# Performance work log

Measured on AMD Instinct MI355X. Metric: run time of the kernel, lower is better.

## Reference

```python
import jax, jax.numpy as jnp
import numpy as np

N = 131072          # source points
M = 65536           # sampled (query) points
NN = 32             # max_nr_neighbors
K = 15              # num_kernel_points
IN_F = 64
OUT_F = 128
MAP_SIZE = 40.0
SUB_DIST = 0.5      # subsampling_dist * subsampling_factor (meters)
KERNEL_RADIUS = max(1.5, 2.0 * SUB_DIST) / MAP_SIZE          # 0.0375
KP_EXTENT = KERNEL_RADIUS / (K ** (1.0 / 3.0) - 1.0) * 1.5
NEG_SLOPE = 0.01    # nn.LeakyReLU default


def setup_inputs() -> dict:
    rng = np.random.RandomState(0)
    points = rng.rand(N, 3).astype(np.float32)

    # ---- gridSampling (faithful numpy port of the torch code) ----
    resolution = SUB_DIST / MAP_SIZE
    grid = np.floor(points / resolution)
    center = (grid + 0.5) * resolution
    dist = ((points - center) ** 2).sum(1)
    dist = dist / dist.max() * 0.7
    v_size = np.ceil(1.0 / resolution)
    grid_idx = grid[:, 0] + grid[:, 1] * v_size + grid[:, 2] * v_size * v_size
    grid_d = grid_idx + dist
    order = np.argsort(grid_d, kind='stable')
    gi_sorted = grid_idx[order]
    first = np.ones(N, bool)
    first[1:] = gi_sorted[1:] != gi_sorted[:-1]
    sample_idx = order[first]  # closest-to-voxel-center point per voxel
    if sample_idx.shape[0] < M:
        sample_idx = np.tile(sample_idx, int(np.ceil(M / sample_idx.shape[0])))
    sample_idx = np.sort(sample_idx[:M])

    # ---- radius search (stand-in for octree.radiusSearchIndices) ----
    # candidates = window in voxel-sorted order, filtered by true euclidean radius,
    # nearest-first, padded with shadow index N (standard KPConv padding).
    pos_in_sorted = np.empty(N, np.int64)
    pos_in_sorted[order] = np.arange(N)
    qpos = pos_in_sorted[sample_idx]
    offs = np.arange(-48, 48)
    cand_pos = np.clip(qpos[:, None] + offs[None, :], 0, N - 1)
    cand_idx = order[cand_pos]                                  # [M,96]
    d2 = ((points[cand_idx] - points[sample_idx][:, None, :]) ** 2).sum(-1)
    valid = d2 <= KERNEL_RADIUS ** 2
    d2w = np.where(valid, d2, np.inf)
    sel = np.argsort(d2w, axis=1)[:, :NN]
    nbr = np.take_along_axis(cand_idx, sel, 1)
    nbr_ok = np.take_along_axis(valid, sel, 1)
    neighbors_index = np.where(nbr_ok, nbr, N).astype(np.int32)  # [M,NN]

    # ---- kernel point dispositions (rigid KPConv buffer) ----
    kp_dir = rng.randn(K, 3).astype(np.float32)
    kp_dir /= np.linalg.norm(kp_dir, axis=1, keepdims=True) + 1e-9
    kernel_points = kp_dir * (rng.rand(K, 1).astype(np.float32) ** (1.0 / 3.0)) * KERNEL_RADIUS

    key = jax.random.key(0)
    ks = jax.random.split(key, 6)
    def lin(k, i, o):
        return (jax.random.normal(k, (i, o), jnp.float32) / np.sqrt(i)).astype(jnp.float32)

    return {
        'points': jnp.asarray(points),
        'features': jax.random.normal(ks[0], (N, IN_F), jnp.float32),
        'W_pre': lin(ks[1], IN_F, OUT_F),
        'b_pre': jnp.zeros((OUT_F,), jnp.float32),
        'kernel_points': jnp.asarray(kernel_points),
        'kp_weights': jax.random.normal(ks[2], (K, OUT_F, OUT_F), jnp.float32) / np.sqrt(K * OUT_F),
        'W_post': lin(ks[3], OUT_F, OUT_F),
        'b_post': jnp.zeros((OUT_F,), jnp.float32),
        'W_sc': lin(ks[4], IN_F, OUT_F),
        'b_sc': jnp.zeros((OUT_F,), jnp.float32),
        'sample_idx': jnp.asarray(sample_idx, jnp.int32),
        'neighbors_index': jnp.asarray(neighbors_index),
    }


def _leaky(x):
    return jnp.where(x >= 0, x, NEG_SLOPE * x)


def reference(points, features, W_pre, b_pre, kernel_points, kp_weights,
              W_post, b_post, W_sc, b_sc, sample_idx, neighbors_index):
    # preactivation: Linear + LeakyReLU (batchnorm=False)
    feats = _leaky(features @ W_pre + b_pre)                       # [N, OUT_F]

    # shadow padding: far point + zero feature row at index N
    s_pts = jnp.concatenate([points, jnp.full((1, 3), 1e6, points.dtype)], 0)
    x_pad = jnp.concatenate([feats, jnp.zeros((1, OUT_F), feats.dtype)], 0)

    # rigid KPConv: gather -> distance influence -> weight -> aggregate
    q_pts = points[sample_idx]                                     # [M,3]
    neighb = s_pts[neighbors_index] - q_pts[:, None, :]            # [M,NN,3]
    sq_d = jnp.sum((neighb[:, :, None, :] - kernel_points[None, None]) ** 2, -1)  # [M,NN,K]
    all_w = jnp.maximum(1.0 - jnp.sqrt(sq_d) / KP_EXTENT, 0.0)     # linear influence
    nx = x_pad[neighbors_index]                                    # [M,NN,OUT_F]
    wfeat = jnp.einsum('mnk,mnc->mkc', all_w, nx)                  # [M,K,OUT_F]
    conv = jnp.einsum('mkc,kco->mo', wfeat, kp_weights)            # [M,OUT_F]

    # post layer: LeakyReLU then Linear (batchnorm=False, relu=True)
    post = _leaky(conv) @ W_post + b_post

    # shortcut on sampled input features (in_fdim != out_fdim -> Linear)
    sc = features[sample_idx] @ W_sc + b_sc
    return _leaky(sc + post)                                       # [M,OUT_F]
```

## Files before the change

kernel.cpp:

```cpp
#include <hip/hip_runtime.h>
#include <cmath>

#define NPTS 131072
#define MTOT 65536
#define NNB  32
#define KKP  15
#define INF  64
#define OUTF 128
#define KCDIM 1920
#define ROWB 3840

typedef __attribute__((ext_vector_type(8))) __bf16 bf16x8;
typedef __attribute__((ext_vector_type(8))) unsigned short u16x8;
typedef __attribute__((ext_vector_type(4))) float f32x4;
typedef unsigned int u32;

__device__ __forceinline__ float bf2f(u32 v){ return __builtin_bit_cast(float, v<<16); }
__device__ __forceinline__ u32 f2bf(float f){
  u32 u = __builtin_bit_cast(u32, f);
  return (u + 0x7fffu + ((u>>16)&1u)) >> 16;
}
__device__ __forceinline__ float leaky(float v){ return v >= 0.f ? v : 0.01f*v; }

__device__ __forceinline__ void g2l16(const void* g, void* l){
  __builtin_amdgcn_global_load_lds((const __attribute__((address_space(1))) u32*)g,
                                   (__attribute__((address_space(3))) u32*)l, 16, 0, 0);
}

__global__ __launch_bounds__(256) void k_cvt_67723(
    const float* __restrict__ kpw, const float* __restrict__ wpost,
    const float* __restrict__ wsc, const float* __restrict__ wpre,
    unsigned short* __restrict__ kpwT, unsigned short* __restrict__ wpostT,
    unsigned short* __restrict__ wscT, unsigned short* __restrict__ wpreT)
{
  int tid = blockIdx.x * 256 + threadIdx.x;
  if (tid < OUTF * KCDIM) {
    int o = tid / KCDIM, kc = tid % KCDIM;
    kpwT[tid] = (unsigned short)f2bf(kpw[(size_t)kc * OUTF + o]);
    return;
  }
  int t2 = tid - OUTF * KCDIM;
  if (t2 < OUTF * OUTF) {
    int o = t2 / OUTF, i = t2 % OUTF;
    wpostT[t2] = (unsigned short)f2bf(wpost[i * OUTF + o]);
    return;
  }
  int t3 = t2 - OUTF * OUTF;
  if (t3 < OUTF * INF) {
    int o = t3 / INF, c = t3 % INF;
    wscT[t3] = (unsigned short)f2bf(wsc[c * OUTF + o]);
    return;
  }
  int t4 = t3 - OUTF * INF;
  if (t4 < OUTF * INF) {
    int o = t4 / INF, c = t4 % INF;
    wpreT[t4] = (unsigned short)f2bf(wpre[c * OUTF + o]);
  }
}

__global__ __launch_bounds__(256) void k_pre_67723(
    const float* __restrict__ feat, const unsigned short* __restrict__ wpreT,
    const float* __restrict__ bp, unsigned short* __restrict__ featbf)
{
  const int w = threadIdx.x >> 6, l = threadIdx.x & 63, lr = l & 15, lg = l >> 4;
  const int m0 = blockIdx.x * 128 + w * 32;
  f32x4 acc[2][8];
#pragma unroll
  for (int ot = 0; ot < 8; ot++) {
    float bv = bp[ot*16 + lr];
    f32x4 s = {bv, bv, bv, bv};
    acc[0][ot] = s; acc[1][ot] = s;
  }
  bf16x8 af[2][2];
#pragma unroll
  for (int mi = 0; mi < 2; mi++)
#pragma unroll
  for (int ks = 0; ks < 2; ks++) {
    const float* src = feat + (size_t)(m0 + mi*16 + lr) * INF + ks*32 + lg*8;
    float4 f0 = *(const float4*)src, f1 = *(const float4*)(src + 4);
    u16x8 p;
    p[0]=f2bf(f0.x); p[1]=f2bf(f0.y); p[2]=f2bf(f0.z); p[3]=f2bf(f0.w);
    p[4]=f2bf(f1.x); p[5]=f2bf(f1.y); p[6]=f2bf(f1.z); p[7]=f2bf(f1.w);
    af[mi][ks] = __builtin_bit_cast(bf16x8, p);
  }
#pragma unroll
  for (int ks = 0; ks < 2; ks++)
#pragma unroll
  for (int ot = 0; ot < 8; ot++) {
    bf16x8 b = *(const bf16x8*)(wpreT + (size_t)(ot*16 + lr) * INF + ks*32 + lg*8);
    acc[0][ot] = __builtin_amdgcn_mfma_f32_16x16x32_bf16(af[0][ks], b, acc[0][ot], 0,0,0);
    acc[1][ot] = __builtin_amdgcn_mfma_f32_16x16x32_bf16(af[1][ks], b, acc[1][ot], 0,0,0);
  }
#pragma unroll
  for (int mi = 0; mi < 2; mi++)
#pragma unroll
  for (int ot = 0; ot < 8; ot++)
#pragma unroll
  for (int r = 0; r < 4; r++) {
    int m = m0 + mi*16 + lg*4 + r;
    featbf[(size_t)m * OUTF + ot*16 + lr] = (unsigned short)f2bf(leaky(acc[mi][ot][r]));
  }
}

__global__ __launch_bounds__(256) void k_wfmma_67723(
    const float* __restrict__ points, const float* __restrict__ kp,
    const int* __restrict__ sample_idx, const int* __restrict__ nbr,
    const unsigned short* __restrict__ featbf, unsigned short* __restrict__ wfeat,
    float inv_ext, int mbase, int nwg)
{
  __shared__ float4 meta[16][32];
  const int bid = blockIdx.x;
  const int swb = (bid & 7) * (nwg >> 3) + (bid >> 3);
  const int m0l = swb * 16;
  const int gm0 = mbase + m0l;
  const int t = threadIdx.x;

  for (int e = t; e < 512; e += 256) {
    int s = e >> 5, n = e & 31;
    int gm = gm0 + s;
    int sidx = sample_idx[gm];
    int ni = nbr[(size_t)gm * NNB + n];
    bool valid = ni < NPTS;
    int nic = valid ? ni : 0;
    float qx = points[sidx*3], qy = points[sidx*3+1], qz = points[sidx*3+2];
    float dx = points[nic*3] - qx, dy = points[nic*3+1] - qy, dz = points[nic*3+2] - qz;
    if (!valid) dx = 1e9f;
    meta[s][n] = make_float4(dx, dy, dz, __int_as_float(nic * (OUTF*2)));
  }
  __syncthreads();

  const int l = t & 63, w = t >> 6, lr = l & 15, lg = l >> 4;
  const bool kvalid = lr < KKP;
  const int kk = kvalid ? lr : 0;
  const float kx = kp[kk*3], ky = kp[kk*3+1], kz = kp[kk*3+2];
  const char* fb = (const char*)featbf;
  const f32x4 zero = {0,0,0,0};

  for (int i = 0; i < 4; i++) {
    const int s = w*4 + i;
    float4 mj[8];
#pragma unroll
    for (int j = 0; j < 8; j++) mj[j] = meta[s][lg*8 + j];

    u32 apk[4];
#pragma unroll
    for (int j2 = 0; j2 < 4; j2++) {
      u32 lohi[2];
#pragma unroll
      for (int h = 0; h < 2; h++) {
        float4 m_ = mj[2*j2 + h];
        float ex = m_.x - kx, ey = m_.y - ky, ez = m_.z - kz;
        float d = sqrtf(ex*ex + ey*ey + ez*ez);
        float wv = fmaxf(1.f - d * inv_ext, 0.f);
        lohi[h] = kvalid ? f2bf(wv) : 0u;
      }
      apk[j2] = lohi[0] | (lohi[1] << 16);
    }
    bf16x8 afr = __builtin_bit_cast(bf16x8, apk);

#pragma unroll
    for (int t2 = 0; t2 < 2; t2++) {
      uint2 dj[8];
#pragma unroll
      for (int j = 0; j < 8; j++) {
        u32 off = __builtin_bit_cast(u32, mj[j].w);
        dj[j] = *(const uint2*)(fb + off + t2*128 + lr*8);
      }
      f32x4 D[4];
#pragma unroll
      for (int q = 0; q < 4; q++) {
        u32 b[4];
#pragma unroll
        for (int u = 0; u < 4; u++) {
          u32 w0 = (q < 2) ? dj[2*u].x   : dj[2*u].y;
          u32 w1 = (q < 2) ? dj[2*u+1].x : dj[2*u+1].y;
          b[u] = __builtin_amdgcn_perm(w1, w0, (q & 1) ? 0x07060302u : 0x05040100u);
        }
        D[q] = __builtin_amdgcn_mfma_f32_16x16x32_bf16(
                   afr, __builtin_bit_cast(bf16x8, b), zero, 0,0,0);
      }
#pragma unroll
      for (int r = 0; r < 4; r++) {
        int kr = lg*4 + r;
        if (kr < KKP) {
          uint2 pv;
          pv.x = f2bf(D[0][r]) | (f2bf(D[1][r]) << 16);
          pv.y = f2bf(D[2][r]) | (f2bf(D[3][r]) << 16);
          *(uint2*)((char*)wfeat + (size_t)(m0l + s) * ROWB + kr*256 + t2*128 + lr*8) = pv;
        }
      }
    }
  }
}

__global__ __launch_bounds__(512) void k_conv_67723(
    const unsigned short* __restrict__ wfeat, const unsigned short* __restrict__ kpwT,
    const unsigned short* __restrict__ wpostT, const unsigned short* __restrict__ wscT,
    const float* __restrict__ features, const float* __restrict__ bpost,
    const float* __restrict__ bsc, const int* __restrict__ sample_idx,
    float* __restrict__ out, int mbase)
{
  extern __shared__ char smem[];
  const int t = threadIdx.x, w = t >> 6, l = t & 63, lr = l & 15, lg = l >> 4;
  const int mq = w >> 1, oh = w & 1;
  const int m0 = blockIdx.x * 128;

  f32x4 acc[2][4];
#pragma unroll
  for (int mi = 0; mi < 2; mi++)
#pragma unroll
  for (int ot = 0; ot < 4; ot++) acc[mi][ot] = (f32x4){0,0,0,0};

  const char* arows = (const char*)wfeat + (size_t)m0 * ROWB;
  const char* brows = (const char*)kpwT;

#pragma unroll
  for (int h = 0; h < 2; h++) {
    int c = t + h*512; int row = c >> 3; int col = c & 7;
    int sinner = (col*16) ^ ((row & 7) << 4);
    g2l16(arows + (size_t)row * ROWB + sinner, smem + c*16);
    g2l16(brows + (size_t)row * ROWB + sinner, smem + 16384 + c*16);
  }
  __syncthreads();

  for (int kt = 0; kt < 30; kt++) {
    const int cur = kt & 1;
    const int nxt_off = (cur ^ 1) << 15;
    if (kt < 29) {
      const int kb = (kt + 1) * 128;
#pragma unroll
      for (int h = 0; h < 2; h++) {
        int c = t + h*512; int row = c >> 3; int col = c & 7;
        int sinner = (col*16) ^ ((row & 7) << 4);
        g2l16(arows + (size_t)row * ROWB + kb + sinner, smem + nxt_off + c*16);
        g2l16(brows + (size_t)row * ROWB + kb + sinner, smem + nxt_off + 16384 + c*16);
      }
    }
    const char* Ab = smem + (cur << 15);
    const char* Bb = Ab + 16384;
#pragma unroll
    for (int ks = 0; ks < 2; ks++) {
      bf16x8 af[2];
#pragma unroll
      for (int mi = 0; mi < 2; mi++) {
        int m = mq*32 + mi*16 + lr;
        af[mi] = *(const bf16x8*)(Ab + m*128 + ((ks*64 + lg*16) ^ ((m & 7) << 4)));
      }
#pragma unroll
      for (int ot = 0; ot < 4; ot++) {
        int o = oh*64 + ot*16 + lr;
        bf16x8 bfr = *(const bf16x8*)(Bb + o*128 + ((ks*64 + lg*16) ^ ((o & 7) << 4)));
        acc[0][ot] = __builtin_amdgcn_mfma_f32_16x16x32_bf16(af[0], bfr, acc[0][ot], 0,0,0);
        acc[1][ot] = __builtin_amdgcn_mfma_f32_16x16x32_bf16(af[1], bfr, acc[1][ot], 0,0,0);
      }
    }
    __syncthreads();
  }

  char* a2 = smem;
  char* a3 = smem + 32768;
#pragma unroll
  for (int mi = 0; mi < 2; mi++)
#pragma unroll
  for (int ot = 0; ot < 4; ot++)
#pragma unroll
  for (int r = 0; r < 4; r++) {
    int m = mq*32 + mi*16 + lg*4 + r;
    int o = oh*64 + ot*16 + lr;
    *(unsigned short*)(a2 + m*256 + ((o*2) ^ ((m & 15) << 4))) =
        (unsigned short)f2bf(leaky(acc[mi][ot][r]));
  }
  for (int e = t; e < 1024; e += 512) {
    int r = e >> 3, seg = e & 7;
    int sidx = sample_idx[mbase + m0 + r];
    const float* src = features + (size_t)sidx * INF + seg*8;
    float4 f0 = *(const float4*)src, f1 = *(const float4*)(src + 4);
    uint4 pv = make_uint4(f2bf(f0.x) | (f2bf(f0.y) << 16),
                          f2bf(f0.z) | (f2bf(f0.w) << 16),
                          f2bf(f1.x) | (f2bf(f1.y) << 16),
                          f2bf(f1.z) | (f2bf(f1.w) << 16));
    *(uint4*)(a3 + r*128 + ((seg*16) ^ ((r & 7) << 4))) = pv;
  }
  __syncthreads();

  f32x4 d[2][4];
#pragma unroll
  for (int ot = 0; ot < 4; ot++) {
    float bv = bpost[oh*64 + ot*16 + lr] + bsc[oh*64 + ot*16 + lr];
    f32x4 s = {bv, bv, bv, bv};
    d[0][ot] = s; d[1][ot] = s;
  }
#pragma unroll
  for (int ks = 0; ks < 4; ks++) {
    bf16x8 af[2];
#pragma unroll
    for (int mi = 0; mi < 2; mi++) {
      int m = mq*32 + mi*16 + lr;
      af[mi] = *(const bf16x8*)(a2 + m*256 + ((ks*64 + lg*16) ^ ((m & 15) << 4)));
    }
#pragma unroll
    for (int ot = 0; ot < 4; ot++) {
      bf16x8 b = *(const bf16x8*)(wpostT + (size_t)(oh*64 + ot*16 + lr) * OUTF + ks*32 + lg*8);
      d[0][ot] = __builtin_amdgcn_mfma_f32_16x16x32_bf16(af[0], b, d[0][ot], 0,0,0);
      d[1][ot] = __builtin_amdgcn_mfma_f32_16x16x32_bf16(af[1], b, d[1][ot], 0,0,0);
    }
  }
#pragma unroll
  for (int ks = 0; ks < 2; ks++) {
    bf16x8 af[2];
#pragma unroll
    for (int mi = 0; mi < 2; mi++) {
      int m = mq*32 + mi*16 + lr;
      af[mi] = *(const bf16x8*)(a3 + m*128 + ((ks*64 + lg*16) ^ ((m & 7) << 4)));
    }
#pragma unroll
    for (int ot = 0; ot < 4; ot++) {
      bf16x8 b = *(const bf16x8*)(wscT + (size_t)(oh*64 + ot*16 + lr) * INF + ks*32 + lg*8);
      d[0][ot] = __builtin_amdgcn_mfma_f32_16x16x32_bf16(af[0], b, d[0][ot], 0,0,0);
      d[1][ot] = __builtin_amdgcn_mfma_f32_16x16x32_bf16(af[1], b, d[1][ot], 0,0,0);
    }
  }
#pragma unroll
  for (int mi = 0; mi < 2; mi++)
#pragma unroll
  for (int ot = 0; ot < 4; ot++)
#pragma unroll
  for (int r = 0; r < 4; r++) {
    int m = mq*32 + mi*16 + lg*4 + r;
    int o = oh*64 + ot*16 + lr;
    out[(size_t)(mbase + m0 + m) * OUTF + o] = leaky(d[mi][ot][r]);
  }
}

extern "C" void kernel_launch(void* const* d_in, const int* in_sizes, int n_in,
                              void* d_out, int out_size, void* d_ws, size_t ws_size,
                              hipStream_t stream)
{
  const float* points   = (const float*)d_in[0];
  const float* features = (const float*)d_in[1];
  const float* W_pre    = (const float*)d_in[2];
  const float* b_pre    = (const float*)d_in[3];
  const float* kpts     = (const float*)d_in[4];
  const float* kpw      = (const float*)d_in[5];
  const float* W_post   = (const float*)d_in[6];
  const float* b_post   = (const float*)d_in[7];
  const float* W_sc     = (const float*)d_in[8];
  const float* b_sc     = (const float*)d_in[9];
  const int* sample_idx = (const int*)d_in[10];
  const int* nbr        = (const int*)d_in[11];
  float* out = (float*)d_out;

  char* ws = (char*)d_ws;
  unsigned short* featbf = (unsigned short*)ws;
  unsigned short* kpwT   = (unsigned short*)(ws + 33554432);
  unsigned short* wpostT = (unsigned short*)(ws + 34045952);
  unsigned short* wscT   = (unsigned short*)(ws + 34078720);
  unsigned short* wpreT  = (unsigned short*)(ws + 34095104);
  unsigned short* wfeat  = (unsigned short*)(ws + 34111488);

  double ext = (1.5 / 40.0) / (pow(15.0, 1.0 / 3.0) - 1.0) * 1.5;
  float inv_ext = (float)(1.0 / ext);

  size_t fixed = 34111488ull;
  int chunks = 1;
  while (chunks < 32 && fixed + 251658240ull / (size_t)chunks > ws_size) chunks <<= 1;
  int msz = MTOT / chunks;

  (void)hipFuncSetAttribute((const void*)k_conv_67723,
                            hipFuncAttributeMaxDynamicSharedMemorySize, 65536);

  k_cvt_67723<<<1088, 256, 0, stream>>>(kpw, W_post, W_sc, W_pre, kpwT, wpostT, wscT, wpreT);
  k_pre_67723<<<1024, 256, 0, stream>>>(features, wpreT, b_pre, featbf);
  for (int ci = 0; ci < chunks; ci++) {
    int nwg = msz / 16;
    k_wfmma_67723<<<nwg, 256, 0, stream>>>(points, kpts, sample_idx, nbr, featbf,
                                           wfeat, inv_ext, ci*msz, nwg);
    k_conv_67723<<<msz/128, 512, 65536, stream>>>(wfeat, kpwT, wpostT, wscT, features,
                                                  b_post, b_sc, sample_idx, out, ci*msz);
  }
}
```

Measured before the change: 167.5 us.

## Fuse weighted-feature aggregation and KP conv GEMM into one LDS-resident kernel

Merges the neighbor-aggregation kernel and the conv/post/shortcut GEMM kernel into a single kernel. Each 512-thread block handles 32 query points and keeps their [32,1920] bf16 weighted-feature tile in LDS (~152KB), streaming only the kernel-point weights from global with double buffering. This removes the large wfeat write and read through HBM and the chunking loop. In exchange, each block covers fewer rows, so the kpwT weights are reloaded once per 32 rows instead of per 128. The large LDS footprint also limits occupancy to one block per CU.

```diff
diff --git a/kernel.cpp b/kernel.cpp
--- a/kernel.cpp
+++ b/kernel.cpp
@@ -9,6 +9,11 @@
 #define OUTF 128
 #define KCDIM 1920
 #define ROWB 3840
+
+#define WF_BYTES   122880
+#define DBUF0_OFF  122880
+#define DBUF1_OFF  139264
+#define LDS_TOTAL  155648
 
 typedef __attribute__((ext_vector_type(8))) __bf16 bf16x8;
 typedef __attribute__((ext_vector_type(8))) unsigned short u16x8;
@@ -102,22 +107,32 @@
   }
 }
 
-__global__ __launch_bounds__(256) void k_wfmma_67723(
-    const float* __restrict__ points, const float* __restrict__ kp,
-    const int* __restrict__ sample_idx, const int* __restrict__ nbr,
-    const unsigned short* __restrict__ featbf, unsigned short* __restrict__ wfeat,
-    float inv_ext, int mbase, int nwg)
+__global__ __launch_bounds__(512) void k_fused_67723(
+    const float* __restrict__ points, const float* __restrict__ features,
+    const float* __restrict__ kp, const float* __restrict__ bpost,
+    const float* __restrict__ bsc, const int* __restrict__ sample_idx,
+    const int* __restrict__ nbr, const unsigned short* __restrict__ featbf,
+    const unsigned short* __restrict__ kpwT, const unsigned short* __restrict__ wpostT,
+    const unsigned short* __restrict__ wscT, float* __restrict__ out,
+    float inv_ext, int nwg)
 {
-  __shared__ float4 meta[16][32];
+  extern __shared__ char smem[];
+  float4* meta = (float4*)(smem + DBUF1_OFF);
+  const int t = threadIdx.x, l = t & 63, w = t >> 6, lr = l & 15, lg = l >> 4;
   const int bid = blockIdx.x;
   const int swb = (bid & 7) * (nwg >> 3) + (bid >> 3);
-  const int m0l = swb * 16;
-  const int gm0 = mbase + m0l;
-  const int t = threadIdx.x;
-
-  for (int e = t; e < 512; e += 256) {
+  const int m0 = swb * 32;
+  const char* brows = (const char*)kpwT;
+
+#pragma unroll
+  for (int h = 0; h < 2; h++) {
+    int c = t + h*512; int row = c >> 3; int col = c & 7;
+    int sinner = (col*16) ^ ((row & 7) << 4);
+    g2l16(brows + (size_t)row * ROWB + sinner, smem + DBUF0_OFF + c*16);
+  }
+  for (int e = t; e < 1024; e += 512) {
     int s = e >> 5, n = e & 31;
-    int gm = gm0 + s;
+    int gm = m0 + s;
     int sidx = sample_idx[gm];
     int ni = nbr[(size_t)gm * NNB + n];
     bool valid = ni < NPTS;
@@ -125,154 +140,123 @@
     float qx = points[sidx*3], qy = points[sidx*3+1], qz = points[sidx*3+2];
     float dx = points[nic*3] - qx, dy = points[nic*3+1] - qy, dz = points[nic*3+2] - qz;
     if (!valid) dx = 1e9f;
-    meta[s][n] = make_float4(dx, dy, dz, __int_as_float(nic * (OUTF*2)));
+    meta[s*32 + n] = make_float4(dx, dy, dz, __int_as_float(nic * (OUTF*2)));
   }
   __syncthreads();
 
-  const int l = t & 63, w = t >> 6, lr = l & 15, lg = l >> 4;
-  const bool kvalid = lr < KKP;
-  const int kk = kvalid ? lr : 0;
-  const float kx = kp[kk*3], ky = kp[kk*3+1], kz = kp[kk*3+2];
-  const char* fb = (const char*)featbf;
-  const f32x4 zero = {0,0,0,0};
-
-  for (int i = 0; i < 4; i++) {
-    const int s = w*4 + i;
-    float4 mj[8];
-#pragma unroll
-    for (int j = 0; j < 8; j++) mj[j] = meta[s][lg*8 + j];
-
-    u32 apk[4];
-#pragma unroll
-    for (int j2 = 0; j2 < 4; j2++) {
-      u32 lohi[2];
-#pragma unroll
-      for (int h = 0; h < 2; h++) {
-        float4 m_ = mj[2*j2 + h];
-        float ex = m_.x - kx, ey = m_.y - ky, ez = m_.z - kz;
-        float d = sqrtf(ex*ex + ey*ey + ez*ez);
-        float wv = fmaxf(1.f - d * inv_ext, 0.f);
-        lohi[h] = kvalid ? f2bf(wv) : 0u;
+  {
+    const bool kvalid = lr < KKP;
+    const int kk = kvalid ? lr : 0;
+    const float kx = kp[kk*3], ky = kp[kk*3+1], kz = kp[kk*3+2];
+    const char* fb = (const char*)featbf;
+    const f32x4 zero = {0,0,0,0};
+    for (int i = 0; i < 4; i++) {
+      const int s = w*4 + i;
+      float4 mj[8];
+#pragma unroll
+      for (int j = 0; j < 8; j++) mj[j] = meta[s*32 + lg*8 + j];
+
+      u32 apk[4];
+#pragma unroll
+      for (int j2 = 0; j2 < 4; j2++) {
+        u32 lohi[2];
+#pragma unroll
+        for (int h = 0; h < 2; h++) {
+          float4 m_ = mj[2*j2 + h];
+          float ex = m_.x - kx, ey = m_.y - ky, ez = m_.z - kz;
+          float d = sqrtf(ex*ex + ey*ey + ez*ez);
+          float wv = fmaxf(1.f - d * inv_ext, 0.f);
+          lohi[h] = kvalid ? f2bf(wv) : 0u;
+        }
+        apk[j2] = lohi[0] | (lohi[1] << 16);
       }
-      apk[j2] = lohi[0] | (lohi[1] << 16);
-    }
-    bf16x8 afr = __builtin_bit_cast(bf16x8, apk);
-
-#pragma unroll
-    for (int t2 = 0; t2 < 2; t2++) {
-      uint2 dj[8];
-#pragma unroll
-      for (int j = 0; j < 8; j++) {
-        u32 off = __builtin_bit_cast(u32, mj[j].w);
-        dj[j] = *(const uint2*)(fb + off + t2*128 + lr*8);
-      }
-      f32x4 D[4];
-#pragma unroll
-      for (int q = 0; q < 4; q++) {
-        u32 b[4];
-#pragma unroll
-        for (int u = 0; u < 4; u++) {
-          u32 w0 = (q < 2) ? dj[2*u].x   : dj[2*u].y;
-          u32 w1 = (q < 2) ? dj[2*u+1].x : dj[2*u+1].y;
-          b[u] = __builtin_amdgcn_perm(w1, w0, (q & 1) ? 0x07060302u : 0x05040100u);
+      bf16x8 afr = __builtin_bit_cast(bf16x8, apk);
+      char* wrow = smem + s * ROWB;
+      const int sswz = (s & 7) << 4;
+
+#pragma unroll
+      for (int t2 = 0; t2 < 2; t2++) {
+        uint2 dj[8];
+#pragma unroll
+        for (int j = 0; j < 8; j++) {
+          u32 off = __builtin_bit_cast(u32, mj[j].w);
+          dj[j] = *(const uint2*)(fb + off + t2*128 + lr*8);
         }
-        D[q] = __builtin_amdgcn_mfma_f32_16x16x32_bf16(
-                   afr, __builtin_bit_cast(bf16x8, b), zero, 0,0,0);
-      }
-#pragma unroll
-      for (int r = 0; r < 4; r++) {
-        int kr = lg*4 + r;
-        if (kr < KKP) {
-          uint2 pv;
-          pv.x = f2bf(D[0][r]) | (f2bf(D[1][r]) << 16);
-          pv.y = f2bf(D[2][r]) | (f2bf(D[3][r]) << 16);
-          *(uint2*)((char*)wfeat + (size_t)(m0l + s) * ROWB + kr*256 + t2*128 + lr*8) = pv;
+        f32x4 D[4];
+#pragma unroll
+        for (int q = 0; q < 4; q++) {
+          u32 b[4];
+#pragma unroll
+          for (int u = 0; u < 4; u++) {
+            u32 w0 = (q < 2) ? dj[2*u].x   : dj[2*u].y;
+            u32 w1 = (q < 2) ? dj[2*u+1].x : dj[2*u+1].y;
+            b[u] = __builtin_amdgcn_perm(w1, w0, (q & 1) ? 0x07060302u : 0x05040100u);
+          }
+          D[q] = __builtin_amdgcn_mfma_f32_16x16x32_bf16(
+                     afr, __builtin_bit_cast(bf16x8, b), zero, 0,0,0);
+        }
+#pragma unroll
+        for (int r = 0; r < 4; r++) {
+          int kr = lg*4 + r;
+          if (kr < KKP) {
+            uint2 pv;
+            pv.x = f2bf(D[0][r]) | (f2bf(D[1][r]) << 16);
+            pv.y = f2bf(D[2][r]) | (f2bf(D[3][r]) << 16);
+            *(uint2*)(wrow + ((kr*256 + t2*128 + lr*8) ^ sswz)) = pv;
+          }
         }
       }
     }
   }
-}
-
-__global__ __launch_bounds__(512) void k_conv_67723(
-    const unsigned short* __restrict__ wfeat, const unsigned short* __restrict__ kpwT,
-    const unsigned short* __restrict__ wpostT, const unsigned short* __restrict__ wscT,
-    const float* __restrict__ features, const float* __restrict__ bpost,
-    const float* __restrict__ bsc, const int* __restrict__ sample_idx,
-    float* __restrict__ out, int mbase)
-{
-  extern __shared__ char smem[];
-  const int t = threadIdx.x, w = t >> 6, l = t & 63, lr = l & 15, lg = l >> 4;
-  const int mq = w >> 1, oh = w & 1;
-  const int m0 = blockIdx.x * 128;
-
-  f32x4 acc[2][4];
-#pragma unroll
-  for (int mi = 0; mi < 2; mi++)
-#pragma unroll
-  for (int ot = 0; ot < 4; ot++) acc[mi][ot] = (f32x4){0,0,0,0};
-
-  const char* arows = (const char*)wfeat + (size_t)m0 * ROWB;
-  const char* brows = (const char*)kpwT;
-
-#pragma unroll
-  for (int h = 0; h < 2; h++) {
-    int c = t + h*512; int row = c >> 3; int col = c & 7;
-    int sinner = (col*16) ^ ((row & 7) << 4);
-    g2l16(arows + (size_t)row * ROWB + sinner, smem + c*16);
-    g2l16(brows + (size_t)row * ROWB + sinner, smem + 16384 + c*16);
-  }
   __syncthreads();
 
+  const int mt = w & 1, oq = w >> 1;
+  const int mrow = mt*16 + lr;
+  const char* arow = smem + mrow * ROWB;
+  const int aswz = (mrow & 7) << 4;
+
+  f32x4 acc[2];
+  acc[0] = (f32x4){0,0,0,0}; acc[1] = (f32x4){0,0,0,0};
+
   for (int kt = 0; kt < 30; kt++) {
-    const int cur = kt & 1;
-    const int nxt_off = (cur ^ 1) << 15;
+    const char* Bb = smem + ((kt & 1) ? DBUF1_OFF : DBUF0_OFF);
     if (kt < 29) {
       const int kb = (kt + 1) * 128;
+      char* dst = smem + (((kt + 1) & 1) ? DBUF1_OFF : DBUF0_OFF);
 #pragma unroll
       for (int h = 0; h < 2; h++) {
         int c = t + h*512; int row = c >> 3; int col = c & 7;
         int sinner = (col*16) ^ ((row & 7) << 4);
-        g2l16(arows + (size_t)row * ROWB + kb + sinner, smem + nxt_off + c*16);
-        g2l16(brows + (size_t)row * ROWB + kb + sinner, smem + nxt_off + 16384 + c*16);
+        g2l16(brows + (size_t)row * ROWB + kb + sinner, dst + c*16);
       }
     }
-    const char* Ab = smem + (cur << 15);
-    const char* Bb = Ab + 16384;
 #pragma unroll
     for (int ks = 0; ks < 2; ks++) {
-      bf16x8 af[2];
-#pragma unroll
-      for (int mi = 0; mi < 2; mi++) {
-        int m = mq*32 + mi*16 + lr;
-        af[mi] = *(const bf16x8*)(Ab + m*128 + ((ks*64 + lg*16) ^ ((m & 7) << 4)));
+      bf16x8 af = *(const bf16x8*)(arow + ((kt*128 + ks*64 + lg*16) ^ aswz));
+#pragma unroll
+      for (int ot = 0; ot < 2; ot++) {
+        int o = oq*32 + ot*16 + lr;
+        bf16x8 bfr = *(const bf16x8*)(Bb + o*128 + ((ks*64 + lg*16) ^ ((o & 7) << 4)));
+        acc[ot] = __builtin_amdgcn_mfma_f32_16x16x32_bf16(af, bfr, acc[ot], 0,0,0);
       }
-#pragma unroll
-      for (int ot = 0; ot < 4; ot++) {
-        int o = oh*64 + ot*16 + lr;
-        bf16x8 bfr = *(const bf16x8*)(Bb + o*128 + ((ks*64 + lg*16) ^ ((o & 7) << 4)));
-        acc[0][ot] = __builtin_amdgcn_mfma_f32_16x16x32_bf16(af[0], bfr, acc[0][ot], 0,0,0);
-        acc[1][ot] = __builtin_amdgcn_mfma_f32_16x16x32_bf16(af[1], bfr, acc[1][ot], 0,0,0);
-      }
     }
     __syncthreads();
   }
 
   char* a2 = smem;
-  char* a3 = smem + 32768;
-#pragma unroll
-  for (int mi = 0; mi < 2; mi++)
-#pragma unroll
-  for (int ot = 0; ot < 4; ot++)
+  char* a3 = smem + 8192;
+#pragma unroll
+  for (int ot = 0; ot < 2; ot++)
 #pragma unroll
   for (int r = 0; r < 4; r++) {
-    int m = mq*32 + mi*16 + lg*4 + r;
-    int o = oh*64 + ot*16 + lr;
+    int m = mt*16 + lg*4 + r;
+    int o = oq*32 + ot*16 + lr;
     *(unsigned short*)(a2 + m*256 + ((o*2) ^ ((m & 15) << 4))) =
-        (unsigned short)f2bf(leaky(acc[mi][ot][r]));
-  }
-  for (int e = t; e < 1024; e += 512) {
-    int r = e >> 3, seg = e & 7;
-    int sidx = sample_idx[mbase + m0 + r];
+        (unsigned short)f2bf(leaky(acc[ot][r]));
+  }
+  if (t < 256) {
+    int r = t >> 3, seg = t & 7;
+    int sidx = sample_idx[m0 + r];
     const float* src = features + (size_t)sidx * INF + seg*8;
     float4 f0 = *(const float4*)src, f1 = *(const float4*)(src + 4);
     uint4 pv = make_uint4(f2bf(f0.x) | (f2bf(f0.y) << 16),
@@ -283,52 +267,37 @@
   }
   __syncthreads();
 
-  f32x4 d[2][4];
-#pragma unroll
-  for (int ot = 0; ot < 4; ot++) {
-    float bv = bpost[oh*64 + ot*16 + lr] + bsc[oh*64 + ot*16 + lr];
-    f32x4 s = {bv, bv, bv, bv};
-    d[0][ot] = s; d[1][ot] = s;
+  f32x4 d[2];
+#pragma unroll
+  for (int ot = 0; ot < 2; ot++) {
+    float bv = bpost[oq*32 + ot*16 + lr] + bsc[oq*32 + ot*16 + lr];
+    d[ot] = (f32x4){bv, bv, bv, bv};
   }
 #pragma unroll
   for (int ks = 0; ks < 4; ks++) {
-    bf16x8 af[2];
-#pragma unroll
-    for (int mi = 0; mi < 2; mi++) {
-      int m = mq*32 + mi*16 + lr;
-      af[mi] = *(const bf16x8*)(a2 + m*256 + ((ks*64 + lg*16) ^ ((m & 15) << 4)));
-    }
-#pragma unroll
-    for (int ot = 0; ot < 4; ot++) {
-      bf16x8 b = *(const bf16x8*)(wpostT + (size_t)(oh*64 + ot*16 + lr) * OUTF + ks*32 + lg*8);
-      d[0][ot] = __builtin_amdgcn_mfma_f32_16x16x32_bf16(af[0], b, d[0][ot], 0,0,0);
-      d[1][ot] = __builtin_amdgcn_mfma_f32_16x16x32_bf16(af[1], b, d[1][ot], 0,0,0);
+    bf16x8 af = *(const bf16x8*)(a2 + mrow*256 + ((ks*64 + lg*16) ^ ((mrow & 15) << 4)));
+#pragma unroll
+    for (int ot = 0; ot < 2; ot++) {
+      bf16x8 b = *(const bf16x8*)(wpostT + (size_t)(oq*32 + ot*16 + lr) * OUTF + ks*32 + lg*8);
+      d[ot] = __builtin_amdgcn_mfma_f32_16x16x32_bf16(af, b, d[ot], 0,0,0);
     }
   }
 #pragma unroll
   for (int ks = 0; ks < 2; ks++) {
-    bf16x8 af[2];
-#pragma unroll
-    for (int mi = 0; mi < 2; mi++) {
-      int m = mq*32 + mi*16 + lr;
-      af[mi] = *(const bf16x8*)(a3 + m*128 + ((ks*64 + lg*16) ^ ((m & 7) << 4)));
-    }
-#pragma unroll
-    for (int ot = 0; ot < 4; ot++) {
-      bf16x8 b = *(const bf16x8*)(wscT + (size_t)(oh*64 + ot*16 + lr) * INF + ks*32 + lg*8);
-      d[0][ot] = __builtin_amdgcn_mfma_f32_16x16x32_bf16(af[0], b, d[0][ot], 0,0,0);
-      d[1][ot] = __builtin_amdgcn_mfma_f32_16x16x32_bf16(af[1], b, d[1][ot], 0,0,0);
-    }
-  }
-#pragma unroll
-  for (int mi = 0; mi < 2; mi++)
-#pragma unroll
-  for (int ot = 0; ot < 4; ot++)
+    bf16x8 af = *(const bf16x8*)(a3 + mrow*128 + ((ks*64 + lg*16) ^ ((mrow & 7) << 4)));
+#pragma unroll
+    for (int ot = 0; ot < 2; ot++) {
+      bf16x8 b = *(const bf16x8*)(wscT + (size_t)(oq*32 + ot*16 + lr) * INF + ks*32 + lg*8);
+      d[ot] = __builtin_amdgcn_mfma_f32_16x16x32_bf16(af, b, d[ot], 0,0,0);
+    }
+  }
+#pragma unroll
+  for (int ot = 0; ot < 2; ot++)
 #pragma unroll
   for (int r = 0; r < 4; r++) {
-    int m = mq*32 + mi*16 + lg*4 + r;
-    int o = oh*64 + ot*16 + lr;
-    out[(size_t)(mbase + m0 + m) * OUTF + o] = leaky(d[mi][ot][r]);
+    int m = mt*16 + lg*4 + r;
+    int o = oq*32 + ot*16 + lr;
+    out[(size_t)(m0 + m) * OUTF + o] = leaky(d[ot][r]);
   }
 }
 
@@ -356,26 +325,17 @@
   unsigned short* wpostT = (unsigned short*)(ws + 34045952);
   unsigned short* wscT   = (unsigned short*)(ws + 34078720);
   unsigned short* wpreT  = (unsigned short*)(ws + 34095104);
-  unsigned short* wfeat  = (unsigned short*)(ws + 34111488);
 
   double ext = (1.5 / 40.0) / (pow(15.0, 1.0 / 3.0) - 1.0) * 1.5;
   float inv_ext = (float)(1.0 / ext);
 
-  size_t fixed = 34111488ull;
-  int chunks = 1;
-  while (chunks < 32 && fixed + 251658240ull / (size_t)chunks > ws_size) chunks <<= 1;
-  int msz = MTOT / chunks;
-
-  (void)hipFuncSetAttribute((const void*)k_conv_67723,
-                            hipFuncAttributeMaxDynamicSharedMemorySize, 65536);
-
+  (void)hipFuncSetAttribute((const void*)k_fused_67723,
+                            hipFuncAttributeMaxDynamicSharedMemorySize, LDS_TOTAL);
+
+  const int nwg = MTOT / 32;
   k_cvt_67723<<<1088, 256, 0, stream>>>(kpw, W_post, W_sc, W_pre, kpwT, wpostT, wscT, wpreT);
   k_pre_67723<<<1024, 256, 0, stream>>>(features, wpreT, b_pre, featbf);
-  for (int ci = 0; ci < chunks; ci++) {
-    int nwg = msz / 16;
-    k_wfmma_67723<<<nwg, 256, 0, stream>>>(points, kpts, sample_idx, nbr, featbf,
-                                           wfeat, inv_ext, ci*msz, nwg);
-    k_conv_67723<<<msz/128, 512, 65536, stream>>>(wfeat, kpwT, wpostT, wscT, features,
-                                                  b_post, b_sc, sample_idx, out, ci*msz);
-  }
-}
+  k_fused_67723<<<nwg, 512, LDS_TOTAL, stream>>>(points, features, kpts, b_post, b_sc,
+                                                 sample_idx, nbr, featbf, kpwT, wpostT,
+                                                 wscT, out, inv_ext, nwg);
+}
```

Result: slower. 240.3 us (+43.5%).
